# Kernel tuning notes

Measured on AMD Instinct MI355X. Metric: run time of the kernel, lower is better.

The kernel has to match this reference:

```python
import jax, jax.numpy as jnp
import numpy as np

PH, PW = 7, 7            # pooled_height, pooled_width
SCALE = 0.0625           # spatial_scale (stride 16)
NEG = jnp.float32(-1e30)


def _make_rois(key, n, img_w, img_h):
    k1, k2, k3, k4 = jax.random.split(key, 4)
    x1 = jax.random.uniform(k1, (n,), minval=0.0, maxval=img_w * 0.75)
    y1 = jax.random.uniform(k2, (n,), minval=0.0, maxval=img_h * 0.75)
    bw = jax.random.uniform(k3, (n,), minval=32.0, maxval=img_w * 0.25)
    bh = jax.random.uniform(k4, (n,), minval=32.0, maxval=img_h * 0.25)
    z = jnp.zeros((n,), jnp.float32)
    return jnp.stack([z, x1, y1, x1 + bw, y1 + bh], axis=1)


def setup_inputs() -> dict:
    key = jax.random.key(0)
    kf, kr1, kr2 = jax.random.split(key, 3)
    feature_map = jax.random.normal(kf, (1, 128, 56, 56), dtype=jnp.float32)
    img = 56.0 / SCALE  # 896
    rois_1 = _make_rois(kr1, 64, img, img)
    rois_2 = _make_rois(kr2, 64, img, img)
    return {"feature_map": feature_map, "rois_1": rois_1, "rois_2": rois_2}


def _zoom(rois, W, H):
    # round(rois[:,1:]*scale) then clamp only the upper bound, like the torch code
    s = jnp.round(rois[:, 1:] * SCALE).astype(jnp.int32)
    x1 = jnp.where(s[:, 0] >= W, W - 1, s[:, 0])
    y1 = jnp.where(s[:, 1] >= H, H - 1, s[:, 1])
    x2 = jnp.where(s[:, 2] >= W, W - 1, s[:, 2])
    y2 = jnp.where(s[:, 3] >= H, H - 1, s[:, 3])
    return x1, y1, x2, y2


def _box_mask(x1, y1, x2, y2, H, W):
    ys = jnp.arange(H)[None, :, None]
    xs = jnp.arange(W)[None, None, :]
    return ((ys >= y1[:, None, None]) & (ys <= y2[:, None, None]) &
            (xs >= x1[:, None, None]) & (xs <= x2[:, None, None]))


def reference(feature_map, rois_1, rois_2):
    feat = feature_map[0]            # C,H,W
    C, H, W = feat.shape
    x1a, y1a, x2a, y2a = _zoom(rois_1, W, H)
    x1b, y1b, x2b, y2b = _zoom(rois_2, W, H)
    # union box per ROI
    ux1 = jnp.minimum(x1a, x1b); uy1 = jnp.minimum(y1a, y1b)
    ux2 = jnp.maximum(x2a, x2b); uy2 = jnp.maximum(y2a, y2b)
    h = uy2 - uy1 + 1                # [B] union heights
    w = ux2 - ux1 + 1                # [B] union widths
    # dual mask: 1 inside either roi (absolute coords), 0 elsewhere
    mask = (_box_mask(x1a, y1a, x2a, y2a, H, W) |
            _box_mask(x1b, y1b, x2b, y2b, H, W)).astype(feat.dtype)  # B,H,W
    val = feat[None, :, :, :] * mask[:, None, :, :]                   # B,C,H,W
    # adaptive max pool bins over the union box: start=floor(i*h/PH), end=ceil((i+1)*h/PH)
    i = jnp.arange(PH)[None, :]
    j = jnp.arange(PW)[None, :]
    rs = uy1[:, None] + (i * h[:, None]) // PH                        # B,PH (abs, incl)
    re = uy1[:, None] + ((i + 1) * h[:, None] + PH - 1) // PH         # B,PH (abs, excl)
    cs = ux1[:, None] + (j * w[:, None]) // PW                        # B,PW
    ce = ux1[:, None] + ((j + 1) * w[:, None] + PW - 1) // PW
    ys = jnp.arange(H)
    xs = jnp.arange(W)
    Ry = (ys[None, None, :] >= rs[:, :, None]) & (ys[None, None, :] < re[:, :, None])  # B,PH,H
    Cx = (xs[None, None, :] >= cs[:, :, None]) & (xs[None, None, :] < ce[:, :, None])  # B,PW,W
    # reduce over x then y (masked max)
    tmp = jnp.max(jnp.where(Cx[:, None, None, :, :], val[:, :, :, None, :], NEG), axis=-1)  # B,C,H,PW
    out = jnp.max(jnp.where(Ry[:, None, :, None, :],
                            tmp.transpose(0, 1, 3, 2)[:, :, None, :, :], NEG), axis=-1)    # B,C,PH,PW
    return out
```

## Files before the change

### kernel.cpp

```cpp
#include <hip/hip_runtime.h>

#define PH 7
#define PW 7
#define SCALE 0.0625f

#define NB 64
#define NC 128
#define FH 56
#define FW 56

__global__ __launch_bounds__(256) void DualMaskRoIPool_kernel(
    const float* __restrict__ feat,
    const float* __restrict__ rois1,
    const float* __restrict__ rois2,
    float* __restrict__ out)
{
    const int total = NB * NC * PH * PW;
    int tid = blockIdx.x * blockDim.x + threadIdx.x;
    if (tid >= total) return;

    int j = tid % PW;
    int i = (tid / PW) % PH;
    int c = (tid / (PW * PH)) % NC;
    int b = tid / (PW * PH * NC);
    b = __builtin_amdgcn_readfirstlane(b);

    const float* r1 = rois1 + b * 5;
    const float* r2 = rois2 + b * 5;
    int x1a = (int)rintf(r1[1] * SCALE);
    int y1a = (int)rintf(r1[2] * SCALE);
    int x2a = (int)rintf(r1[3] * SCALE);
    int y2a = (int)rintf(r1[4] * SCALE);
    int x1b = (int)rintf(r2[1] * SCALE);
    int y1b = (int)rintf(r2[2] * SCALE);
    int x2b = (int)rintf(r2[3] * SCALE);
    int y2b = (int)rintf(r2[4] * SCALE);
    if (x1a >= FW) x1a = FW - 1;
    if (y1a >= FH) y1a = FH - 1;
    if (x2a >= FW) x2a = FW - 1;
    if (y2a >= FH) y2a = FH - 1;
    if (x1b >= FW) x1b = FW - 1;
    if (y1b >= FH) y1b = FH - 1;
    if (x2b >= FW) x2b = FW - 1;
    if (y2b >= FH) y2b = FH - 1;

    int ux1 = min(x1a, x1b);
    int uy1 = min(y1a, y1b);
    int ux2 = max(x2a, x2b);
    int uy2 = max(y2a, y2b);
    int h = uy2 - uy1 + 1;
    int w = ux2 - ux1 + 1;

    int rs = uy1 + (i * h) / PH;
    int re = uy1 + ((i + 1) * h + PH - 1) / PH;
    int cs = ux1 + (j * w) / PW;
    int ce = ux1 + ((j + 1) * w + PW - 1) / PW;

    const float* fc = feat + c * (FH * FW);
    float m = -1e30f;
    for (int y = rs; y < re; ++y) {
        bool iny1 = (y >= y1a) && (y <= y2a);
        bool iny2 = (y >= y1b) && (y <= y2b);
        const float* frow = fc + y * FW;
        for (int x = cs; x < ce; ++x) {
            bool in = (iny1 && (x >= x1a) && (x <= x2a)) ||
                      (iny2 && (x >= x1b) && (x <= x2b));
            float v = in ? frow[x] : 0.0f;
            m = fmaxf(m, v);
        }
    }
    out[tid] = m;
}

extern "C" void kernel_launch(void* const* d_in, const int* in_sizes, int n_in,
                              void* d_out, int out_size, void* d_ws, size_t ws_size,
                              hipStream_t stream) {
    const float* feat  = (const float*)d_in[0];
    const float* rois1 = (const float*)d_in[1];
    const float* rois2 = (const float*)d_in[2];
    float* out = (float*)d_out;

    const int total = NB * NC * PH * PW;
    const int block = 256;
    const int grid = (total + block - 1) / block;
    DualMaskRoIPool_kernel<<<grid, block, 0, stream>>>(feat, rois1, rois2, out);
}
```

Baseline: 69.59 us.

## Remap threads to channels per bin block and skip masked-out loads

```diff
diff --git a/kernel.cpp b/kernel.cpp
--- a/kernel.cpp
+++ b/kernel.cpp
@@ -9,21 +9,17 @@
 #define FH 56
 #define FW 56
 
-__global__ __launch_bounds__(256) void DualMaskRoIPool_kernel(
+__global__ __launch_bounds__(NC) void DualMaskRoIPool_kernel(
     const float* __restrict__ feat,
     const float* __restrict__ rois1,
     const float* __restrict__ rois2,
     float* __restrict__ out)
 {
-    const int total = NB * NC * PH * PW;
-    int tid = blockIdx.x * blockDim.x + threadIdx.x;
-    if (tid >= total) return;
-
-    int j = tid % PW;
-    int i = (tid / PW) % PH;
-    int c = (tid / (PW * PH)) % NC;
-    int b = tid / (PW * PH * NC);
-    b = __builtin_amdgcn_readfirstlane(b);
+    const int c   = threadIdx.x;
+    const int bin = blockIdx.x;
+    const int b   = blockIdx.y;
+    const int i   = bin / PW;
+    const int j   = bin % PW;
 
     const float* r1 = rois1 + b * 5;
     const float* r2 = rois2 + b * 5;
@@ -44,32 +40,36 @@
     if (x2b >= FW) x2b = FW - 1;
     if (y2b >= FH) y2b = FH - 1;
 
-    int ux1 = min(x1a, x1b);
-    int uy1 = min(y1a, y1b);
-    int ux2 = max(x2a, x2b);
-    int uy2 = max(y2a, y2b);
-    int h = uy2 - uy1 + 1;
-    int w = ux2 - ux1 + 1;
+    const int ux1 = min(x1a, x1b);
+    const int uy1 = min(y1a, y1b);
+    const int ux2 = max(x2a, x2b);
+    const int uy2 = max(y2a, y2b);
+    const int h = uy2 - uy1 + 1;
+    const int w = ux2 - ux1 + 1;
 
-    int rs = uy1 + (i * h) / PH;
-    int re = uy1 + ((i + 1) * h + PH - 1) / PH;
-    int cs = ux1 + (j * w) / PW;
-    int ce = ux1 + ((j + 1) * w + PW - 1) / PW;
+    const int rs = uy1 + (i * h) / PH;
+    const int re = uy1 + ((i + 1) * h + PH - 1) / PH;
+    const int cs = ux1 + (j * w) / PW;
+    const int ce = ux1 + ((j + 1) * w + PW - 1) / PW;
 
     const float* fc = feat + c * (FH * FW);
     float m = -1e30f;
+    bool has_zero = false;
     for (int y = rs; y < re; ++y) {
-        bool iny1 = (y >= y1a) && (y <= y2a);
-        bool iny2 = (y >= y1b) && (y <= y2b);
+        const bool iny1 = (y >= y1a) && (y <= y2a);
+        const bool iny2 = (y >= y1b) && (y <= y2b);
+        if (!iny1 && !iny2) { has_zero = true; continue; }
         const float* frow = fc + y * FW;
         for (int x = cs; x < ce; ++x) {
-            bool in = (iny1 && (x >= x1a) && (x <= x2a)) ||
-                      (iny2 && (x >= x1b) && (x <= x2b));
-            float v = in ? frow[x] : 0.0f;
-            m = fmaxf(m, v);
+            const bool in = (iny1 && (x >= x1a) && (x <= x2a)) ||
+                            (iny2 && (x >= x1b) && (x <= x2b));
+            if (in) m = fmaxf(m, frow[x]);
+            else    has_zero = true;
         }
     }
-    out[tid] = m;
+    if (has_zero) m = fmaxf(m, 0.0f);
+
+    out[((b * NC + c) * PH + i) * PW + j] = m;
 }
 
 extern "C" void kernel_launch(void* const* d_in, const int* in_sizes, int n_in,
@@ -80,8 +80,6 @@
     const float* rois2 = (const float*)d_in[2];
     float* out = (float*)d_out;
 
-    const int total = NB * NC * PH * PW;
-    const int block = 256;
-    const int grid = (total + block - 1) / block;
-    DualMaskRoIPool_kernel<<<grid, block, 0, stream>>>(feat, rois1, rois2, out);
+    dim3 grid(PH * PW, NB);
+    DualMaskRoIPool_kernel<<<grid, NC, 0, stream>>>(feat, rois1, rois2, out);
 }
```

New measurement: 72.17 us. +3.7%, slower.
